# Kernel tuning notes

Hardware: AMD Instinct MI355X
Metric: run time of the kernel (lower is better)

Reference implementation:

```python
import jax, jax.numpy as jnp
import numpy as np

EPS = 1e-5
NHEAD = 8

def layernorm(x, g, b):
    m = x.mean(-1, keepdims=True)
    v = ((x - m) ** 2).mean(-1, keepdims=True)
    return (x - m) * jax.lax.rsqrt(v + EPS) * g + b


def setup_inputs() -> dict:
    key = jax.random.key(0)
    ks = jax.random.split(key, 20)
    D, F, K, G, NC, FF, B = 768, 2048, 100, 10, 1000, 2048, 128
    s = lambda k, shape, scale: jax.random.normal(k, shape, jnp.float32) * scale
    return {
        "x": s(ks[0], (B, F, 7, 7), 1.0),
        "W_embed": s(ks[1], (F, D), 0.02), "b_embed": jnp.zeros((D,), jnp.float32),
        "query_embed": s(ks[2], (K, D), 1.0),
        "wq": s(ks[3], (D, D), 0.03), "wk": s(ks[4], (D, D), 0.03), "wv": s(ks[5], (D, D), 0.03),
        "bq": jnp.zeros((D,), jnp.float32), "bk": jnp.zeros((D,), jnp.float32), "bv": jnp.zeros((D,), jnp.float32),
        "wo": s(ks[6], (D, D), 0.03), "bo": jnp.zeros((D,), jnp.float32),
        "w1": s(ks[7], (D, FF), 0.03), "b1": jnp.zeros((FF,), jnp.float32),
        "w2": s(ks[8], (FF, D), 0.02), "b2": jnp.zeros((D,), jnp.float32),
        "g1": jnp.ones((D,), jnp.float32), "be1": jnp.zeros((D,), jnp.float32),
        "g2": jnp.ones((D,), jnp.float32), "be2": jnp.zeros((D,), jnp.float32),
        "g3": jnp.ones((D,), jnp.float32), "be3": jnp.zeros((D,), jnp.float32),
        "dup_pool": s(ks[9], (K, D, G), 0.03),
        "dup_bias": jnp.zeros((NC,), jnp.float32),
    }


def reference(x, W_embed, b_embed, query_embed, wq, wk, wv, bq, bk, bv, wo, bo,
              w1, b1, w2, b2, g1, be1, g2, be2, g3, be3, dup_pool, dup_bias):
    B = x.shape[0]
    D = W_embed.shape[1]
    H = NHEAD
    hd = D // H
    num_classes = dup_bias.shape[0]

    # [B, 2048, 7, 7] -> [B, 49, 2048] -> [B, 49, 768], relu
    mem = x.reshape(B, x.shape[1], -1).transpose(0, 2, 1)
    mem = jax.nn.relu(mem @ W_embed + b_embed)          # (B, S, D)

    # queries broadcast to batch (batch-first internally)
    tgt = jnp.broadcast_to(query_embed[None], (B,) + query_embed.shape)  # (B, K, D)

    # tgt = tgt + dropout1(tgt) -> 2*tgt in eval; then norm1
    tgt = layernorm(2.0 * tgt, g1, be1)

    # cross multi-head attention: Q=tgt, K=V=mem
    q = (tgt @ wq + bq).reshape(B, -1, H, hd)
    k = (mem @ wk + bk).reshape(B, -1, H, hd)
    v = (mem @ wv + bv).reshape(B, -1, H, hd)
    scores = jnp.einsum("bkhd,bshd->bhks", q, k) / jnp.sqrt(jnp.float32(hd))
    attn = jax.nn.softmax(scores, axis=-1)
    ctx = jnp.einsum("bhks,bshd->bkhd", attn, v).reshape(B, -1, D)
    attn_out = ctx @ wo + bo

    tgt = layernorm(tgt + attn_out, g2, be2)

    # FFN
    ff = jax.nn.relu(tgt @ w1 + b1) @ w2 + b2
    h = layernorm(tgt + ff, g3, be3)                    # (B, K, D)

    # GroupFC: per-group matmul, batched as one einsum
    out_extrap = jnp.einsum("bkd,kdg->bkg", h, dup_pool)  # (B, K, G)
    logits = out_extrap.reshape(B, -1)[:, :num_classes] + dup_bias
    return logits
```

## Files before the change

### kernel.cpp

```cpp
#include <hip/hip_runtime.h>
#include <math.h>

#define D_MODEL 768
#define HEADS   8
#define HDIM    96
#define SEQ     49
#define KQ      100
#define NB      128
#define FDIM    2048
#define FFD     2048
#define GRP     10
#define NCLS    1000

typedef unsigned short ushort_t;
typedef unsigned int uint_t;
typedef __attribute__((ext_vector_type(8))) short short8;
typedef __attribute__((ext_vector_type(4))) float f32x4;

__device__ __forceinline__ float bf2f(ushort_t u) {
    uint_t x = ((uint_t)u) << 16;
    return __uint_as_float(x);
}
__device__ __forceinline__ ushort_t f2bf(float f) {
    uint_t x = __float_as_uint(f);
    x += 0x7fffu + ((x >> 16) & 1u);
    return (ushort_t)(x >> 16);
}

__device__ __forceinline__ void gld_lds16(const void* g, void* l) {
    __builtin_amdgcn_global_load_lds(
        (const __attribute__((address_space(1))) unsigned int*)g,
        (__attribute__((address_space(3))) unsigned int*)l, 16, 0, 0);
}

template <int MT>
__global__ __launch_bounds__(256, (MT == 2 ? 4 : 3)) void gemm_bf16(
    const ushort_t* __restrict__ A, const ushort_t* __restrict__ Bt,
    const float* __restrict__ bias, const float* __restrict__ bias2,
    ushort_t* __restrict__ C, ushort_t* __restrict__ C2,
    int M, int N, int K, int nsplit, int relu, float scale)
{
    constexpr int BM  = MT * 32;
    constexpr int ACH = MT * 4;
    constexpr int NCH = (ACH + 16) / 4;

    __shared__ ushort_t As[BM * 64];
    __shared__ ushort_t Bs[128 * 64];

    const int tid  = threadIdx.x;
    const int w    = tid >> 6;
    const int lane = tid & 63;
    const int quad = lane >> 4;
    const int l16  = lane & 15;
    const int rowBase = blockIdx.y * BM;
    const int nBase   = blockIdx.x * 128;
    const int wr = (w >> 1) * (MT * 16);
    const int wc = (w & 1) * 64;

    const float* biasb;
    ushort_t* Cb;
    int coff, ldcb;
    if (nBase < nsplit) { biasb = bias;  Cb = C;  coff = 0;      ldcb = nsplit; }
    else                { biasb = bias2; Cb = C2; coff = nsplit; ldcb = N - nsplit; }

    f32x4 acc[MT][4];
#pragma unroll
    for (int i = 0; i < MT; i++)
#pragma unroll
        for (int j = 0; j < 4; j++) acc[i][j] = (f32x4){0.f, 0.f, 0.f, 0.f};

    const int lrow = lane >> 3;
    const int ksub = ((lane & 7) ^ ((lane >> 3) & 7)) * 8;

    const ushort_t* gp[NCH];
    ushort_t* lp[NCH];
#pragma unroll
    for (int i = 0; i < NCH; i++) {
        int c = w + 4 * i;
        if (c < ACH) {
            int r = min(rowBase + c * 8 + lrow, M - 1);
            gp[i] = A + (size_t)r * K + ksub;
            lp[i] = As + c * 512 + lane * 8;
        } else {
            int cb = c - ACH;
            int r = nBase + cb * 8 + lrow;
            gp[i] = Bt + (size_t)r * K + ksub;
            lp[i] = Bs + cb * 512 + lane * 8;
        }
    }

    const int swl = l16 & 7;

    for (int k0 = 0; k0 < K; k0 += 64) {
#pragma unroll
        for (int i = 0; i < NCH; i++) gld_lds16(gp[i] + k0, lp[i]);
        __syncthreads();

#pragma unroll
        for (int s = 0; s < 2; s++) {
            const int ks = ((4 * s + quad) ^ swl) * 8;
            short8 af[MT], bfr[4];
#pragma unroll
            for (int mt = 0; mt < MT; mt++)
                af[mt] = *(const short8*)(As + (wr + mt * 16 + l16) * 64 + ks);
#pragma unroll
            for (int nt = 0; nt < 4; nt++)
                bfr[nt] = *(const short8*)(Bs + (wc + nt * 16 + l16) * 64 + ks);
#pragma unroll
            for (int mt = 0; mt < MT; mt++)
#pragma unroll
                for (int nt = 0; nt < 4; nt++)
                    acc[mt][nt] = __builtin_amdgcn_mfma_f32_16x16x32_bf16(
                        af[mt], bfr[nt], acc[mt][nt], 0, 0, 0);
        }
        __syncthreads();
    }

#pragma unroll
    for (int nt = 0; nt < 4; nt++) {
        const int colg = nBase + wc + nt * 16 + l16;
        const int col  = colg - coff;
        const float bv = biasb[col];
#pragma unroll
        for (int mt = 0; mt < MT; mt++) {
#pragma unroll
            for (int r = 0; r < 4; r++) {
                const int row = rowBase + wr + mt * 16 + quad * 4 + r;
                if (row < M) {
                    float v = (acc[mt][nt][r] + bv) * scale;
                    if (relu) v = fmaxf(v, 0.f);
                    Cb[(size_t)row * ldcb + col] = f2bf(v);
                }
            }
        }
    }
}

__global__ __launch_bounds__(256) void wt_conv_all(
    const float* __restrict__ We, const float* __restrict__ wq,
    const float* __restrict__ wk, const float* __restrict__ wv,
    const float* __restrict__ wo, const float* __restrict__ w1,
    const float* __restrict__ w2,
    ushort_t* __restrict__ Wet, ushort_t* __restrict__ wqt,
    ushort_t* __restrict__ wkt, ushort_t* __restrict__ wvt,
    ushort_t* __restrict__ wot, ushort_t* __restrict__ w1t,
    ushort_t* __restrict__ w2t)
{
    __shared__ float tile[64][65];
    int t = blockIdx.x;
    const float* src; ushort_t* dst; int K, N, tx;
    if (t < 384)       {           src = We; dst = Wet; K = 2048; N = 768;  tx = 12; }
    else if (t < 528)  { t -= 384; src = wq; dst = wqt; K = 768;  N = 768;  tx = 12; }
    else if (t < 672)  { t -= 528; src = wk; dst = wkt; K = 768;  N = 768;  tx = 12; }
    else if (t < 816)  { t -= 672; src = wv; dst = wvt; K = 768;  N = 768;  tx = 12; }
    else if (t < 960)  { t -= 816; src = wo; dst = wot; K = 768;  N = 768;  tx = 12; }
    else if (t < 1344) { t -= 960; src = w1; dst = w1t; K = 768;  N = 2048; tx = 32; }
    else               { t -= 1344; src = w2; dst = w2t; K = 2048; N = 768; tx = 12; }
    const int n0 = (t % tx) * 64, k0 = (t / tx) * 64;
    const int tr = threadIdx.x >> 6, tc = threadIdx.x & 63;
#pragma unroll
    for (int i = 0; i < 16; i++) {
        int r = i * 4 + tr;
        tile[r][tc] = src[(size_t)(k0 + r) * N + n0 + tc];
    }
    __syncthreads();
#pragma unroll
    for (int i = 0; i < 16; i++) {
        int nr = i * 4 + tr;
        dst[(size_t)(n0 + nr) * K + k0 + tc] = f2bf(tile[tc][nr]);
    }
}

__global__ __launch_bounds__(256) void x_conv(
    const float* __restrict__ x, ushort_t* __restrict__ xb)
{
    __shared__ ushort_t tile[256][50];
    const int b = blockIdx.y, f0 = blockIdx.x * 256, t = threadIdx.x;
    const float* src = x + ((size_t)b * FDIM + f0 + t) * SEQ;
#pragma unroll
    for (int s = 0; s < SEQ; s++) tile[t][s] = f2bf(src[s]);
    __syncthreads();
    for (int s = 0; s < SEQ; s++)
        xb[(size_t)(b * SEQ + s) * FDIM + f0 + t] = tile[t][s];
}

__device__ __forceinline__ float block_reduce_sum_f(float v, float* red)
{
#pragma unroll
    for (int off = 32; off > 0; off >>= 1) v += __shfl_down(v, off);
    int lane = threadIdx.x & 63, w = threadIdx.x >> 6;
    if (lane == 0) red[w] = v;
    __syncthreads();
    float total = red[0] + red[1] + red[2] + red[3];
    __syncthreads();
    return total;
}

__global__ __launch_bounds__(256) void ln_fused(
    const void* __restrict__ in, int in_bf16,
    const ushort_t* __restrict__ resid, int rmode,
    const float* __restrict__ g, const float* __restrict__ be,
    ushort_t* __restrict__ out, float pre_scale)
{
    __shared__ float red[4];
    const int row = blockIdx.x;
    const int tid = threadIdx.x;

    float v[3];
#pragma unroll
    for (int i = 0; i < 3; i++) {
        int d = tid + i * 256;
        float x;
        if (in_bf16) x = bf2f(((const ushort_t*)in)[(size_t)row * D_MODEL + d]);
        else         x = ((const float*)in)[(size_t)row * D_MODEL + d];
        x *= pre_scale;
        if (rmode == 1)      x += bf2f(resid[(size_t)row * D_MODEL + d]);
        else if (rmode == 2) x += bf2f(resid[(size_t)(row % KQ) * D_MODEL + d]);
        v[i] = x;
    }
    float s = block_reduce_sum_f(v[0] + v[1] + v[2], red);
    float mean = s * (1.f / D_MODEL);
    float d0 = v[0] - mean, d1 = v[1] - mean, d2 = v[2] - mean;
    float sq = block_reduce_sum_f(d0 * d0 + d1 * d1 + d2 * d2, red);
    float rstd = rsqrtf(sq * (1.f / D_MODEL) + 1e-5f);
#pragma unroll
    for (int i = 0; i < 3; i++) {
        int d = tid + i * 256;
        out[(size_t)row * D_MODEL + d] = f2bf((v[i] - mean) * rstd * g[d] + be[d]);
    }
}

__global__ __launch_bounds__(256) void attn_mfma(
    const ushort_t* __restrict__ q, const ushort_t* __restrict__ k,
    const ushort_t* __restrict__ v, ushort_t* __restrict__ ctx)
{
    __shared__ ushort_t Pt[128][72];
    __shared__ ushort_t Vt[96][72];

    const int bh = blockIdx.x;
    const int b = bh >> 3, h = bh & 7;
    const int tid = threadIdx.x;
    const int w = tid >> 6, lane = tid & 63;
    const int quad = lane >> 4, l16 = lane & 15;
    const int mrow0 = 32 * w;

    for (int idx = tid; idx < 96 * 64; idx += 256) {
        int d = idx >> 6, s = idx & 63;
        ushort_t val = 0;
        if (s < SEQ) val = v[(size_t)(b * SEQ + s) * D_MODEL + h * HDIM + d];
        Vt[d][s] = val;
    }

    f32x4 accS[2][4];
#pragma unroll
    for (int i = 0; i < 2; i++)
#pragma unroll
        for (int j = 0; j < 4; j++) accS[i][j] = (f32x4){0.f, 0.f, 0.f, 0.f};

#pragma unroll
    for (int k0 = 0; k0 < HDIM; k0 += 32) {
        short8 af[2], bfr[4];
#pragma unroll
        for (int mt = 0; mt < 2; mt++) {
            int kq = min(mrow0 + mt * 16 + l16, KQ - 1);
            af[mt] = *(const short8*)(q + (size_t)kq * D_MODEL + h * HDIM + k0 + quad * 8);
        }
#pragma unroll
        for (int nt = 0; nt < 4; nt++) {
            int s = min(nt * 16 + l16, SEQ - 1);
            bfr[nt] = *(const short8*)(k + (size_t)(b * SEQ + s) * D_MODEL + h * HDIM + k0 + quad * 8);
        }
#pragma unroll
        for (int mt = 0; mt < 2; mt++)
#pragma unroll
            for (int nt = 0; nt < 4; nt++)
                accS[mt][nt] = __builtin_amdgcn_mfma_f32_16x16x32_bf16(
                    af[mt], bfr[nt], accS[mt][nt], 0, 0, 0);
    }

#pragma unroll
    for (int mt = 0; mt < 2; mt++) {
#pragma unroll
        for (int r = 0; r < 4; r++) {
            float vals[4];
            float vmax = -1e30f;
#pragma unroll
            for (int nt = 0; nt < 4; nt++) {
                vals[nt] = accS[mt][nt][r];
                if (nt * 16 + l16 < SEQ) vmax = fmaxf(vmax, vals[nt]);
            }
#pragma unroll
            for (int off = 1; off < 16; off <<= 1)
                vmax = fmaxf(vmax, __shfl_xor(vmax, off));
            float p[4], psum = 0.f;
#pragma unroll
            for (int nt = 0; nt < 4; nt++) {
                float e = (nt * 16 + l16 < SEQ) ? __expf(vals[nt] - vmax) : 0.f;
                p[nt] = e;
                psum += e;
            }
#pragma unroll
            for (int off = 1; off < 16; off <<= 1)
                psum += __shfl_xor(psum, off);
            const float inv = 1.f / psum;
            const int row = mrow0 + mt * 16 + quad * 4 + r;
#pragma unroll
            for (int nt = 0; nt < 4; nt++)
                Pt[row][nt * 16 + l16] = f2bf(p[nt] * inv);
        }
    }
    __syncthreads();

    f32x4 accO[2][6];
#pragma unroll
    for (int i = 0; i < 2; i++)
#pragma unroll
        for (int j = 0; j < 6; j++) accO[i][j] = (f32x4){0.f, 0.f, 0.f, 0.f};

#pragma unroll
    for (int k0 = 0; k0 < 64; k0 += 32) {
        short8 af[2], bfr[6];
#pragma unroll
        for (int mt = 0; mt < 2; mt++)
            af[mt] = *(const short8*)(&Pt[mrow0 + mt * 16 + l16][k0 + quad * 8]);
#pragma unroll
        for (int nt = 0; nt < 6; nt++)
            bfr[nt] = *(const short8*)(&Vt[nt * 16 + l16][k0 + quad * 8]);
#pragma unroll
        for (int mt = 0; mt < 2; mt++)
#pragma unroll
            for (int nt = 0; nt < 6; nt++)
                accO[mt][nt] = __builtin_amdgcn_mfma_f32_16x16x32_bf16(
                    af[mt], bfr[nt], accO[mt][nt], 0, 0, 0);
    }

#pragma unroll
    for (int mt = 0; mt < 2; mt++) {
#pragma unroll
        for (int r = 0; r < 4; r++) {
            const int kq = mrow0 + mt * 16 + quad * 4 + r;
            if (kq < KQ) {
                size_t oa = (size_t)(b * KQ + kq) * D_MODEL + h * HDIM;
#pragma unroll
                for (int nt = 0; nt < 6; nt++)
                    ctx[oa + nt * 16 + l16] = f2bf(accO[mt][nt][r]);
            }
        }
    }
}

__global__ __launch_bounds__(256) void groupfc2(
    const ushort_t* __restrict__ h, const float* __restrict__ dp,
    const float* __restrict__ dbias, float* __restrict__ out)
{
    __shared__ float dps[D_MODEL * 11];
    __shared__ float hsr[8][D_MODEL];

    const int b0 = blockIdx.x * 8;
    const int kq = blockIdx.y;
    const int tid = threadIdx.x;

    for (int i = tid; i < D_MODEL * GRP; i += 256) {
        int d = i / GRP, g = i - d * GRP;
        dps[d * 11 + g] = dp[(size_t)kq * (D_MODEL * GRP) + i];
    }
#pragma unroll
    for (int bb = 0; bb < 8; bb++) {
#pragma unroll
        for (int i = 0; i < 3; i++) {
            int d = tid + i * 256;
            hsr[bb][d] = bf2f(h[(size_t)((b0 + bb) * KQ + kq) * D_MODEL + d]);
        }
    }
    __syncthreads();

    const int w = tid >> 6, lane = tid & 63;
    for (int item = w; item < 8 * GRP; item += 4) {
        int bb = item / GRP, g = item - bb * GRP;
        float a = 0.f;
#pragma unroll
        for (int i = 0; i < 12; i++) {
            int d = lane + i * 64;
            a = fmaf(hsr[bb][d], dps[d * 11 + g], a);
        }
#pragma unroll
        for (int off = 32; off > 0; off >>= 1) a += __shfl_down(a, off);
        if (lane == 0)
            out[(size_t)(b0 + bb) * NCLS + kq * GRP + g] = a + dbias[kq * GRP + g];
    }
}

extern "C" void kernel_launch(void* const* d_in, const int* in_sizes, int n_in,
                              void* d_out, int out_size, void* d_ws, size_t ws_size,
                              hipStream_t stream)
{
    const float* x   = (const float*)d_in[0];
    const float* We  = (const float*)d_in[1];
    const float* be_ = (const float*)d_in[2];
    const float* qe  = (const float*)d_in[3];
    const float* wq  = (const float*)d_in[4];
    const float* wk  = (const float*)d_in[5];
    const float* wv  = (const float*)d_in[6];
    const float* bq  = (const float*)d_in[7];
    const float* bk  = (const float*)d_in[8];
    const float* bv  = (const float*)d_in[9];
    const float* wo  = (const float*)d_in[10];
    const float* bo  = (const float*)d_in[11];
    const float* w1  = (const float*)d_in[12];
    const float* b1  = (const float*)d_in[13];
    const float* w2  = (const float*)d_in[14];
    const float* b2  = (const float*)d_in[15];
    const float* g1  = (const float*)d_in[16];
    const float* be1 = (const float*)d_in[17];
    const float* g2  = (const float*)d_in[18];
    const float* be2 = (const float*)d_in[19];
    const float* g3  = (const float*)d_in[20];
    const float* be3 = (const float*)d_in[21];
    const float* dp  = (const float*)d_in[22];
    const float* db  = (const float*)d_in[23];
    float* out = (float*)d_out;
    ushort_t* ws = (ushort_t*)d_ws;

    ushort_t* xb  = ws;
    ushort_t* mem = xb + 12845056;
    ushort_t* kb  = mem + 4816896;
    ushort_t* vb  = kb + 4816896;
    ushort_t* ffh = ws;
    ushort_t* rB  = ws + 27295744;
    ushort_t* Wet = rB;
    ushort_t* wqt = Wet + 1572864;
    ushort_t* wkt = wqt + 589824;
    ushort_t* wvt = wkt + 589824;
    ushort_t* wot = wvt + 589824;
    ushort_t* w1t = wot + 589824;
    ushort_t* w2t = w1t + 1572864;
    ushort_t* tgt = w2t + 1572864;
    ushort_t* qb  = tgt + 76800;
    ushort_t* ctx = qb + 76800;
    ushort_t* t2  = ctx + 9830400;
    ushort_t* hb  = t2 + 9830400;

    dim3 blk(256);
    const float qscale = 1.0f / sqrtf((float)HDIM);

    x_conv<<<dim3(8, NB), blk, 0, stream>>>(x, xb);
    wt_conv_all<<<dim3(1728), blk, 0, stream>>>(We, wq, wk, wv, wo, w1, w2,
                                                Wet, wqt, wkt, wvt, wot, w1t, w2t);

    gemm_bf16<2><<<dim3(6, 98), blk, 0, stream>>>(xb, Wet, be_, be_, mem, mem,
                                                  6272, 768, 2048, 768, 1, 1.f);
    ln_fused<<<dim3(KQ), blk, 0, stream>>>(qe, 0, nullptr, 0, g1, be1, tgt, 2.0f);
    gemm_bf16<4><<<dim3(6, 1), blk, 0, stream>>>(tgt, wqt, bq, bq, qb, qb,
                                                 KQ, 768, 768, 768, 0, qscale);
    gemm_bf16<4><<<dim3(12, 49), blk, 0, stream>>>(mem, wkt, bk, bv, kb, vb,
                                                   6272, 1536, 768, 768, 0, 1.f);
    attn_mfma<<<dim3(NB * HEADS), blk, 0, stream>>>(qb, kb, vb, ctx);
    gemm_bf16<4><<<dim3(6, 100), blk, 0, stream>>>(ctx, wot, bo, bo, t2, t2,
                                                   12800, 768, 768, 768, 0, 1.f);
    ln_fused<<<dim3(12800), blk, 0, stream>>>(t2, 1, tgt, 2, g2, be2, t2, 1.0f);
    gemm_bf16<4><<<dim3(16, 100), blk, 0, stream>>>(t2, w1t, b1, b1, ffh, ffh,
                                                    12800, 2048, 768, 2048, 1, 1.f);
    gemm_bf16<4><<<dim3(6, 100), blk, 0, stream>>>(ffh, w2t, b2, b2, hb, hb,
                                                   12800, 768, 2048, 768, 0, 1.f);
    ln_fused<<<dim3(12800), blk, 0, stream>>>(hb, 1, t2, 1, g3, be3, hb, 1.0f);
    groupfc2<<<dim3(16, KQ), blk, 0, stream>>>(hb, dp, db, out);
}
```

Baseline: 544.8 us.

## Fuse residual adds into GEMM epilogues, merge prep kernels, fold final LN into GroupFC

Residual additions move into the epilogue of the output-projection and FFN-down GEMMs. The final layernorm is folded into the GroupFC kernel, and the x and weight conversion kernels are merged into one launch. LayerNorm is rewritten as one wavefront per row with packed loads, and the Q projection uses a smaller M tile. GEMM launch bounds are raised to 4 waves per SIMD for all tile sizes, which may cause register spills for MT=4.

```diff
diff --git a/kernel.cpp b/kernel.cpp
--- a/kernel.cpp
+++ b/kernel.cpp
@@ -34,11 +34,12 @@
 }
 
 template <int MT>
-__global__ __launch_bounds__(256, (MT == 2 ? 4 : 3)) void gemm_bf16(
+__global__ __launch_bounds__(256, 4) void gemm_bf16(
     const ushort_t* __restrict__ A, const ushort_t* __restrict__ Bt,
     const float* __restrict__ bias, const float* __restrict__ bias2,
     ushort_t* __restrict__ C, ushort_t* __restrict__ C2,
-    int M, int N, int K, int nsplit, int relu, float scale)
+    int M, int N, int K, int nsplit, int relu, float scale,
+    const ushort_t* __restrict__ resid, int rmode)
 {
     constexpr int BM  = MT * 32;
     constexpr int ACH = MT * 4;
@@ -129,6 +130,10 @@
                 if (row < M) {
                     float v = (acc[mt][nt][r] + bv) * scale;
                     if (relu) v = fmaxf(v, 0.f);
+                    if (rmode) {
+                        int rrow = (rmode == 2) ? (row % KQ) : row;
+                        v += bf2f(resid[(size_t)rrow * D_MODEL + col]);
+                    }
                     Cb[(size_t)row * ldcb + col] = f2bf(v);
                 }
             }
@@ -136,97 +141,104 @@
     }
 }
 
-__global__ __launch_bounds__(256) void wt_conv_all(
+__global__ __launch_bounds__(256) void prep_all(
     const float* __restrict__ We, const float* __restrict__ wq,
     const float* __restrict__ wk, const float* __restrict__ wv,
     const float* __restrict__ wo, const float* __restrict__ w1,
-    const float* __restrict__ w2,
+    const float* __restrict__ w2, const float* __restrict__ x,
     ushort_t* __restrict__ Wet, ushort_t* __restrict__ wqt,
     ushort_t* __restrict__ wkt, ushort_t* __restrict__ wvt,
     ushort_t* __restrict__ wot, ushort_t* __restrict__ w1t,
-    ushort_t* __restrict__ w2t)
+    ushort_t* __restrict__ w2t, ushort_t* __restrict__ xb)
 {
-    __shared__ float tile[64][65];
+    __shared__ __align__(16) char smem[25600];
     int t = blockIdx.x;
-    const float* src; ushort_t* dst; int K, N, tx;
-    if (t < 384)       {           src = We; dst = Wet; K = 2048; N = 768;  tx = 12; }
-    else if (t < 528)  { t -= 384; src = wq; dst = wqt; K = 768;  N = 768;  tx = 12; }
-    else if (t < 672)  { t -= 528; src = wk; dst = wkt; K = 768;  N = 768;  tx = 12; }
-    else if (t < 816)  { t -= 672; src = wv; dst = wvt; K = 768;  N = 768;  tx = 12; }
-    else if (t < 960)  { t -= 816; src = wo; dst = wot; K = 768;  N = 768;  tx = 12; }
-    else if (t < 1344) { t -= 960; src = w1; dst = w1t; K = 768;  N = 2048; tx = 32; }
-    else               { t -= 1344; src = w2; dst = w2t; K = 2048; N = 768; tx = 12; }
-    const int n0 = (t % tx) * 64, k0 = (t / tx) * 64;
-    const int tr = threadIdx.x >> 6, tc = threadIdx.x & 63;
-#pragma unroll
-    for (int i = 0; i < 16; i++) {
-        int r = i * 4 + tr;
-        tile[r][tc] = src[(size_t)(k0 + r) * N + n0 + tc];
-    }
-    __syncthreads();
-#pragma unroll
-    for (int i = 0; i < 16; i++) {
-        int nr = i * 4 + tr;
-        dst[(size_t)(n0 + nr) * K + k0 + tc] = f2bf(tile[tc][nr]);
-    }
-}
-
-__global__ __launch_bounds__(256) void x_conv(
-    const float* __restrict__ x, ushort_t* __restrict__ xb)
+    if (t < 1728) {
+        float* tile = (float*)smem;
+        const float* src; ushort_t* dst; int K, N, tx;
+        if (t < 384)       {           src = We; dst = Wet; K = 2048; N = 768;  tx = 12; }
+        else if (t < 528)  { t -= 384; src = wq; dst = wqt; K = 768;  N = 768;  tx = 12; }
+        else if (t < 672)  { t -= 528; src = wk; dst = wkt; K = 768;  N = 768;  tx = 12; }
+        else if (t < 816)  { t -= 672; src = wv; dst = wvt; K = 768;  N = 768;  tx = 12; }
+        else if (t < 960)  { t -= 816; src = wo; dst = wot; K = 768;  N = 768;  tx = 12; }
+        else if (t < 1344) { t -= 960; src = w1; dst = w1t; K = 768;  N = 2048; tx = 32; }
+        else               { t -= 1344; src = w2; dst = w2t; K = 2048; N = 768; tx = 12; }
+        const int n0 = (t % tx) * 64, k0 = (t / tx) * 64;
+        const int tr = threadIdx.x >> 6, tc = threadIdx.x & 63;
+#pragma unroll
+        for (int i = 0; i < 16; i++) {
+            int r = i * 4 + tr;
+            tile[r * 65 + tc] = src[(size_t)(k0 + r) * N + n0 + tc];
+        }
+        __syncthreads();
+#pragma unroll
+        for (int i = 0; i < 16; i++) {
+            int nr = i * 4 + tr;
+            dst[(size_t)(n0 + nr) * K + k0 + tc] = f2bf(tile[tc * 65 + nr]);
+        }
+    } else {
+        ushort_t* tile = (ushort_t*)smem;
+        int bx = t - 1728;
+        const int b = bx >> 3, f0 = (bx & 7) * 256, tt = threadIdx.x;
+        const float* src = x + ((size_t)b * FDIM + f0 + tt) * SEQ;
+#pragma unroll
+        for (int s = 0; s < SEQ; s++) tile[tt * 50 + s] = f2bf(src[s]);
+        __syncthreads();
+        for (int s = 0; s < SEQ; s++)
+            xb[(size_t)(b * SEQ + s) * FDIM + f0 + tt] = tile[tt * 50 + s];
+    }
+}
+
+__global__ __launch_bounds__(256) void ln4(
+    const void* __restrict__ in, int in_bf16,
+    const float* __restrict__ g, const float* __restrict__ be,
+    ushort_t* __restrict__ out, float pre_scale, int nrows)
 {
-    __shared__ ushort_t tile[256][50];
-    const int b = blockIdx.y, f0 = blockIdx.x * 256, t = threadIdx.x;
-    const float* src = x + ((size_t)b * FDIM + f0 + t) * SEQ;
-#pragma unroll
-    for (int s = 0; s < SEQ; s++) tile[t][s] = f2bf(src[s]);
-    __syncthreads();
-    for (int s = 0; s < SEQ; s++)
-        xb[(size_t)(b * SEQ + s) * FDIM + f0 + t] = tile[t][s];
-}
-
-__device__ __forceinline__ float block_reduce_sum_f(float v, float* red)
-{
-#pragma unroll
-    for (int off = 32; off > 0; off >>= 1) v += __shfl_down(v, off);
-    int lane = threadIdx.x & 63, w = threadIdx.x >> 6;
-    if (lane == 0) red[w] = v;
-    __syncthreads();
-    float total = red[0] + red[1] + red[2] + red[3];
-    __syncthreads();
-    return total;
-}
-
-__global__ __launch_bounds__(256) void ln_fused(
-    const void* __restrict__ in, int in_bf16,
-    const ushort_t* __restrict__ resid, int rmode,
-    const float* __restrict__ g, const float* __restrict__ be,
-    ushort_t* __restrict__ out, float pre_scale)
-{
-    __shared__ float red[4];
-    const int row = blockIdx.x;
-    const int tid = threadIdx.x;
-
-    float v[3];
-#pragma unroll
-    for (int i = 0; i < 3; i++) {
-        int d = tid + i * 256;
-        float x;
-        if (in_bf16) x = bf2f(((const ushort_t*)in)[(size_t)row * D_MODEL + d]);
-        else         x = ((const float*)in)[(size_t)row * D_MODEL + d];
-        x *= pre_scale;
-        if (rmode == 1)      x += bf2f(resid[(size_t)row * D_MODEL + d]);
-        else if (rmode == 2) x += bf2f(resid[(size_t)(row % KQ) * D_MODEL + d]);
-        v[i] = x;
-    }
-    float s = block_reduce_sum_f(v[0] + v[1] + v[2], red);
-    float mean = s * (1.f / D_MODEL);
-    float d0 = v[0] - mean, d1 = v[1] - mean, d2 = v[2] - mean;
-    float sq = block_reduce_sum_f(d0 * d0 + d1 * d1 + d2 * d2, red);
-    float rstd = rsqrtf(sq * (1.f / D_MODEL) + 1e-5f);
-#pragma unroll
-    for (int i = 0; i < 3; i++) {
-        int d = tid + i * 256;
-        out[(size_t)row * D_MODEL + d] = f2bf((v[i] - mean) * rstd * g[d] + be[d]);
+    const int w = threadIdx.x >> 6, lane = threadIdx.x & 63;
+    const int row = blockIdx.x * 4 + w;
+    if (row >= nrows) return;
+
+    float v[12];
+    if (in_bf16) {
+        const uint_t* p = (const uint_t*)in + (size_t)row * 384;
+#pragma unroll
+        for (int i = 0; i < 6; i++) {
+            uint_t u = p[lane + i * 64];
+            v[2 * i]     = bf2f((ushort_t)(u & 0xffff)) * pre_scale;
+            v[2 * i + 1] = bf2f((ushort_t)(u >> 16)) * pre_scale;
+        }
+    } else {
+        const float2* p = (const float2*)((const float*)in + (size_t)row * D_MODEL);
+#pragma unroll
+        for (int i = 0; i < 6; i++) {
+            float2 t = p[lane + i * 64];
+            v[2 * i] = t.x * pre_scale;
+            v[2 * i + 1] = t.y * pre_scale;
+        }
+    }
+    float s = 0.f;
+#pragma unroll
+    for (int i = 0; i < 12; i++) s += v[i];
+#pragma unroll
+    for (int off = 32; off > 0; off >>= 1) s += __shfl_xor(s, off);
+    const float mean = s * (1.f / D_MODEL);
+    float q = 0.f;
+#pragma unroll
+    for (int i = 0; i < 12; i++) { float d = v[i] - mean; q += d * d; }
+#pragma unroll
+    for (int off = 32; off > 0; off >>= 1) q += __shfl_xor(q, off);
+    const float rstd = rsqrtf(q * (1.f / D_MODEL) + 1e-5f);
+
+    const float2* g2 = (const float2*)g;
+    const float2* b2 = (const float2*)be;
+    uint_t* op = (uint_t*)out + (size_t)row * 384;
+#pragma unroll
+    for (int i = 0; i < 6; i++) {
+        int j = lane + i * 64;
+        float2 gg = g2[j], bb = b2[j];
+        ushort_t lo = f2bf((v[2 * i] - mean) * rstd * gg.x + bb.x);
+        ushort_t hi = f2bf((v[2 * i + 1] - mean) * rstd * gg.y + bb.y);
+        op[j] = (uint_t)lo | ((uint_t)hi << 16);
     }
 }
 
@@ -349,12 +361,14 @@
     }
 }
 
-__global__ __launch_bounds__(256) void groupfc2(
-    const ushort_t* __restrict__ h, const float* __restrict__ dp,
-    const float* __restrict__ dbias, float* __restrict__ out)
+__global__ __launch_bounds__(256) void groupfc3(
+    const ushort_t* __restrict__ hb, const float* __restrict__ dp,
+    const float* __restrict__ dbias, const float* __restrict__ g3,
+    const float* __restrict__ be3, float* __restrict__ out)
 {
     __shared__ float dps[D_MODEL * 11];
     __shared__ float hsr[8][D_MODEL];
+    __shared__ float gbs[2][D_MODEL];
 
     const int b0 = blockIdx.x * 8;
     const int kq = blockIdx.y;
@@ -364,17 +378,46 @@
         int d = i / GRP, g = i - d * GRP;
         dps[d * 11 + g] = dp[(size_t)kq * (D_MODEL * GRP) + i];
     }
+    for (int i = tid; i < D_MODEL; i += 256) {
+        gbs[0][i] = g3[i];
+        gbs[1][i] = be3[i];
+    }
 #pragma unroll
     for (int bb = 0; bb < 8; bb++) {
 #pragma unroll
         for (int i = 0; i < 3; i++) {
             int d = tid + i * 256;
-            hsr[bb][d] = bf2f(h[(size_t)((b0 + bb) * KQ + kq) * D_MODEL + d]);
+            hsr[bb][d] = bf2f(hb[(size_t)((b0 + bb) * KQ + kq) * D_MODEL + d]);
         }
     }
     __syncthreads();
 
     const int w = tid >> 6, lane = tid & 63;
+
+#pragma unroll
+    for (int rr = 0; rr < 2; rr++) {
+        const int r = w * 2 + rr;
+        float v[12];
+        float s = 0.f;
+#pragma unroll
+        for (int i = 0; i < 12; i++) { v[i] = hsr[r][lane + i * 64]; s += v[i]; }
+#pragma unroll
+        for (int off = 32; off > 0; off >>= 1) s += __shfl_xor(s, off);
+        const float mean = s * (1.f / D_MODEL);
+        float q = 0.f;
+#pragma unroll
+        for (int i = 0; i < 12; i++) { float d = v[i] - mean; q += d * d; }
+#pragma unroll
+        for (int off = 32; off > 0; off >>= 1) q += __shfl_xor(q, off);
+        const float rstd = rsqrtf(q * (1.f / D_MODEL) + 1e-5f);
+#pragma unroll
+        for (int i = 0; i < 12; i++) {
+            int d = lane + i * 64;
+            hsr[r][d] = (v[i] - mean) * rstd * gbs[0][d] + gbs[1][d];
+        }
+    }
+    __syncthreads();
+
     for (int item = w; item < 8 * GRP; item += 4) {
         int bb = item / GRP, g = item - bb * GRP;
         float a = 0.f;
@@ -443,25 +486,23 @@
     dim3 blk(256);
     const float qscale = 1.0f / sqrtf((float)HDIM);
 
-    x_conv<<<dim3(8, NB), blk, 0, stream>>>(x, xb);
-    wt_conv_all<<<dim3(1728), blk, 0, stream>>>(We, wq, wk, wv, wo, w1, w2,
-                                                Wet, wqt, wkt, wvt, wot, w1t, w2t);
+    prep_all<<<dim3(2752), blk, 0, stream>>>(We, wq, wk, wv, wo, w1, w2, x,
+                                             Wet, wqt, wkt, wvt, wot, w1t, w2t, xb);
 
     gemm_bf16<2><<<dim3(6, 98), blk, 0, stream>>>(xb, Wet, be_, be_, mem, mem,
-                                                  6272, 768, 2048, 768, 1, 1.f);
-    ln_fused<<<dim3(KQ), blk, 0, stream>>>(qe, 0, nullptr, 0, g1, be1, tgt, 2.0f);
-    gemm_bf16<4><<<dim3(6, 1), blk, 0, stream>>>(tgt, wqt, bq, bq, qb, qb,
-                                                 KQ, 768, 768, 768, 0, qscale);
+                                                  6272, 768, 2048, 768, 1, 1.f, nullptr, 0);
+    ln4<<<dim3(25), blk, 0, stream>>>(qe, 0, g1, be1, tgt, 2.0f, KQ);
+    gemm_bf16<1><<<dim3(6, 4), blk, 0, stream>>>(tgt, wqt, bq, bq, qb, qb,
+                                                 KQ, 768, 768, 768, 0, qscale, nullptr, 0);
     gemm_bf16<4><<<dim3(12, 49), blk, 0, stream>>>(mem, wkt, bk, bv, kb, vb,
-                                                   6272, 1536, 768, 768, 0, 1.f);
+                                                   6272, 1536, 768, 768, 0, 1.f, nullptr, 0);
     attn_mfma<<<dim3(NB * HEADS), blk, 0, stream>>>(qb, kb, vb, ctx);
     gemm_bf16<4><<<dim3(6, 100), blk, 0, stream>>>(ctx, wot, bo, bo, t2, t2,
-                                                   12800, 768, 768, 768, 0, 1.f);
-    ln_fused<<<dim3(12800), blk, 0, stream>>>(t2, 1, tgt, 2, g2, be2, t2, 1.0f);
+                                                   12800, 768, 768, 768, 0, 1.f, tgt, 2);
+    ln4<<<dim3(3200), blk, 0, stream>>>(t2, 1, g2, be2, t2, 1.0f, 12800);
     gemm_bf16<4><<<dim3(16, 100), blk, 0, stream>>>(t2, w1t, b1, b1, ffh, ffh,
-                                                    12800, 2048, 768, 2048, 1, 1.f);
+                                                    12800, 2048, 768, 2048, 1, 1.f, nullptr, 0);
     gemm_bf16<4><<<dim3(6, 100), blk, 0, stream>>>(ffh, w2t, b2, b2, hb, hb,
-                                                   12800, 768, 2048, 768, 0, 1.f);
-    ln_fused<<<dim3(12800), blk, 0, stream>>>(hb, 1, t2, 1, g3, be3, hb, 1.0f);
-    groupfc2<<<dim3(16, KQ), blk, 0, stream>>>(hb, dp, db, out);
-}
+                                                   12800, 768, 2048, 768, 0, 1.f, t2, 1);
+    groupfc3<<<dim3(16, KQ), blk, 0, stream>>>(hb, dp, db, g3, be3, out);
+}
```

After: 537.4 us. About the same (-1.4%).
